# Kernel tuning notes

Hardware: AMD Instinct MI355X
Metric: run time of the kernel (lower is better)

Reference implementation:

```python
import jax, jax.numpy as jnp
import numpy as np

KH, KW, PAD, G = 3, 3, 1, 4  # kernel, padding, deformable groups


def _bilinear_gather(xg, py, px):
    """xg: [B,G,C,Hin,Win]; py,px: [B,G,K,H,W] sample coords.
    Returns [B,G,C,K,H,W] with zero padding outside the image (mmcv semantics)."""
    B, Gd, C, Hin, Win = xg.shape
    y0 = jnp.floor(py)
    x0 = jnp.floor(px)
    wy1 = py - y0
    wx1 = px - x0
    wy0 = 1.0 - wy1
    wx0 = 1.0 - wx1
    xf = xg.reshape(B, Gd, C, Hin * Win)

    def gather(yi, xi):
        valid = (yi >= 0) & (yi < Hin) & (xi >= 0) & (xi < Win)
        yc = jnp.clip(yi, 0, Hin - 1).astype(jnp.int32)
        xc = jnp.clip(xi, 0, Win - 1).astype(jnp.int32)
        lin = (yc * Win + xc).reshape(B, Gd, 1, -1)  # [B,G,1,K*H*W]
        v = jnp.take_along_axis(xf, lin, axis=3).reshape(B, Gd, C, *yi.shape[2:])
        return v * valid[:, :, None].astype(xg.dtype)

    return (gather(y0, x0) * (wy0 * wx0)[:, :, None]
            + gather(y0, x0 + 1) * (wy0 * wx1)[:, :, None]
            + gather(y0 + 1, x0) * (wy1 * wx0)[:, :, None]
            + gather(y0 + 1, x0 + 1) * (wy1 * wx1)[:, :, None])


def setup_inputs() -> dict:
    key = jax.random.key(0)
    k1, k2, k3, k4 = jax.random.split(key, 4)
    B, Cin, Cout, H, W = 8, 256, 256, 64, 64
    x = jax.random.normal(k1, (B, Cin, H, W), dtype=jnp.float32)
    shape = jax.random.normal(k2, (B, 4, H, W), dtype=jnp.float32)
    # conv_offset: 1x1 conv, 4 -> G*2*KH*KW = 72 channels, no bias
    w_offset = jax.random.normal(k3, (G * 2 * KH * KW, 4), dtype=jnp.float32) * 0.1
    # conv_adaption: deform conv weight, no bias
    w_deform = jax.random.normal(k4, (Cout, Cin, KH, KW), dtype=jnp.float32) * 0.01
    return {"x": x, "shape": shape, "w_offset": w_offset, "w_deform": w_deform}


def reference(x, shape, w_offset, w_deform):
    B, Cin, H, W = x.shape
    Cout = w_deform.shape[0]
    K = KH * KW
    # 1x1 offset-predicting conv on detached shape
    shape = jax.lax.stop_gradient(shape)
    offset = jnp.einsum('oc,bchw->bohw', w_offset, shape)  # [B, G*2*K, H, W]
    off = offset.reshape(B, G, K, 2, H, W)  # mmcv layout: (dy, dx) per tap
    dy, dx = off[:, :, :, 0], off[:, :, :, 1]  # [B,G,K,H,W]
    # base sampling grid for each kernel tap
    ky, kx = jnp.meshgrid(jnp.arange(KH), jnp.arange(KW), indexing='ij')
    ky = ky.reshape(-1)
    kx = kx.reshape(-1)
    base_y = (ky - PAD)[:, None, None] + jnp.arange(H)[None, :, None]  # [K,H,1]
    base_x = (kx - PAD)[:, None, None] + jnp.arange(W)[None, None, :]  # [K,1,W]
    py = base_y[None, None].astype(x.dtype) + dy  # [B,G,K,H,W]
    px = base_x[None, None].astype(x.dtype) + dx
    xg = x.reshape(B, G, Cin // G, H, W)
    sampled = _bilinear_gather(xg, py, px)  # [B,G,Cpg,K,H,W]
    wr = w_deform.reshape(Cout, G, Cin // G, K)
    out = jnp.einsum('ogck,bgckhw->bohw', wr, sampled)
    return jax.nn.relu(out)
```

## Files before the change

kernel.cpp:

```cpp
#include <hip/hip_runtime.h>
#include <hip/hip_bf16.h>


#define Bn   8
#define CIN  256
#define COUT 256
#define Hn   64
#define Wn   64
#define Gn   4
#define Kn   9
#define CPG  64
#define GK   36

typedef __bf16 bf16x8 __attribute__((ext_vector_type(8)));
typedef float  f32x4  __attribute__((ext_vector_type(4)));

__global__ void fa_prep(const float* __restrict__ x, const float* __restrict__ w,
                        __bf16* __restrict__ xt, __bf16* __restrict__ wfrag) {
    const int bid = blockIdx.x, t = threadIdx.x;
    if (bid < 4096) {
        const int c8q = bid & 7, hwt = (bid >> 3) & 63, b = bid >> 9;
        const int hw = hwt * 64 + (t & 63);
        const int c8 = c8q * 4 + (t >> 6);
        const float* xp = x + ((size_t)(b * CIN + c8 * 8) << 12) + hw;
        bf16x8 v;
#pragma unroll
        for (int j = 0; j < 8; j++) v[j] = (__bf16)xp[(size_t)j << 12];
        *(bf16x8*)&xt[(((size_t)b << 12) + hw) * 256 + c8 * 8] = v;
    } else {
        int i = (bid - 4096) * 256 + t;
        int j    = i & 7;
        int lane = (i >> 3) & 63;
        int ks   = (i >> 9) & 1;
        int mt   = (i >> 10) & 15;
        int gk   = i >> 14;
        int g = gk / Kn, k = gk - g * Kn;
        int o = mt * 16 + (lane & 15);
        int c = ks * 32 + (lane >> 4) * 8 + j;
        wfrag[i] = (__bf16)w[(size_t)(o * CIN + g * CPG + c) * Kn + k];
    }
}

__global__ __launch_bounds__(256, 2)
void fa_main(const __bf16* __restrict__ xt, const float* __restrict__ shp,
             const float* __restrict__ w_off, const __bf16* __restrict__ wfrag,
             float* __restrict__ out) {
    const int blk = blockIdx.x;
    const int bp = blk >> 7, h = (blk >> 1) & 63, wh = blk & 1;
    const int w0 = wh * 32;
    const int t = threadIdx.x;
    const int wid = t >> 6, lane = t & 63;
    const int col = lane & 15, quad = lane >> 4;
    const int cg = t & 7, nl0 = t >> 3;

    __shared__ int   s_iyx[GK * 64];
    __shared__ float s_fy[GK * 64];
    __shared__ float s_fx[GK * 64];
    __shared__ __align__(16) __bf16 sB[2][64 * 64];

    for (int i = t; i < GK * 64; i += 256) {
        int gk = i >> 6, n = i & 63;
        int bb = n >> 5, w = w0 + (n & 31);
        int b = bp * 2 + bb;
        int g = gk / Kn, k = gk - g * Kn;
        int ky = k / 3, kx = k - ky * 3;
        int oy = (g * Kn + k) * 2;
        float dy = 0.f, dx = 0.f;
#pragma unroll
        for (int c = 0; c < 4; c++) {
            float sv = shp[((b * 4 + c) * Hn + h) * Wn + w];
            dy = fmaf(w_off[(oy    ) * 4 + c], sv, dy);
            dx = fmaf(w_off[(oy + 1) * 4 + c], sv, dx);
        }
        float py = (float)(h + ky - 1) + dy;
        float px = (float)(w + kx - 1) + dx;
        float y0 = floorf(py), x0 = floorf(px);
        s_fy[i] = py - y0;
        s_fx[i] = px - x0;
        s_iyx[i] = (((int)y0 & 0xffff) << 16) | ((int)x0 & 0xffff);
    }

    bf16x8 c4[2][4];
    float  w4[2][4];

    auto issue = [&](int gk) {
#pragma unroll
        for (int s = 0; s < 2; s++) {
            int n = nl0 + s * 32;
            int bb = n >> 5;
            int b = bp * 2 + bb;
            int m = gk * 64 + n;
            int g = gk / Kn;
            int pk = s_iyx[m];
            int iy = pk >> 16, ix = (pk << 16) >> 16;
            float fy = s_fy[m], fx = s_fx[m];
            bool y0v = (unsigned)iy       < (unsigned)Hn;
            bool y1v = (unsigned)(iy + 1) < (unsigned)Hn;
            bool x0v = (unsigned)ix       < (unsigned)Wn;
            bool x1v = (unsigned)(ix + 1) < (unsigned)Wn;
            int yc0 = min(max(iy, 0), Hn - 1), yc1 = min(max(iy + 1, 0), Hn - 1);
            int xc0 = min(max(ix, 0), Wn - 1), xc1 = min(max(ix + 1, 0), Wn - 1);
            const __bf16* base = xt + (((size_t)b << 12)) * 256 + g * CPG + cg * 8;
            c4[s][0] = *(const bf16x8*)(base + ((size_t)(yc0 * 64 + xc0)) * 256);
            c4[s][1] = *(const bf16x8*)(base + ((size_t)(yc0 * 64 + xc1)) * 256);
            c4[s][2] = *(const bf16x8*)(base + ((size_t)(yc1 * 64 + xc0)) * 256);
            c4[s][3] = *(const bf16x8*)(base + ((size_t)(yc1 * 64 + xc1)) * 256);
            float wy1 = fy, wy0 = 1.f - fy, wx1 = fx, wx0 = 1.f - fx;
            w4[s][0] = (y0v && x0v) ? wy0 * wx0 : 0.f;
            w4[s][1] = (y0v && x1v) ? wy0 * wx1 : 0.f;
            w4[s][2] = (y1v && x0v) ? wy1 * wx0 : 0.f;
            w4[s][3] = (y1v && x1v) ? wy1 * wx1 : 0.f;
        }
    };
    auto commit = [&](int buf) {
#pragma unroll
        for (int s = 0; s < 2; s++) {
            int n = nl0 + s * 32;
            bf16x8 r;
#pragma unroll
            for (int j = 0; j < 8; j++) {
                float v = w4[s][0] * (float)c4[s][0][j] + w4[s][1] * (float)c4[s][1][j]
                        + w4[s][2] * (float)c4[s][2][j] + w4[s][3] * (float)c4[s][3][j];
                r[j] = (__bf16)v;
            }
            *(bf16x8*)&sB[buf][(n * 8 + (cg ^ (n & 7))) * 8] = r;
        }
    };

    f32x4 acc[4][4];
#pragma unroll
    for (int mt = 0; mt < 4; mt++)
#pragma unroll
        for (int nt = 0; nt < 4; nt++) acc[mt][nt] = (f32x4){0.f, 0.f, 0.f, 0.f};

    __syncthreads();

    issue(0);
    commit(0);
    issue(1);
    __syncthreads();

    for (int gk = 0; gk < GK; gk++) {
        const int buf = gk & 1;
        const __bf16* wbase = wfrag + (((size_t)gk * 16 + wid * 4) * 2) * 512;
        bf16x8 af[2][4];
#pragma unroll
        for (int ks = 0; ks < 2; ks++)
#pragma unroll
            for (int mt = 0; mt < 4; mt++)
                af[ks][mt] = *(const bf16x8*)(wbase + ((size_t)(mt * 2 + ks) * 64 + lane) * 8);
        if (gk + 1 < GK) commit(buf ^ 1);
        if (gk + 2 < GK) issue(gk + 2);
#pragma unroll
        for (int ks = 0; ks < 2; ks++) {
            bf16x8 bfv[4];
#pragma unroll
            for (int nt = 0; nt < 4; nt++) {
                int n = nt * 16 + col;
                int cq8 = ks * 4 + quad;
                bfv[nt] = *(const bf16x8*)&sB[buf][(n * 8 + (cq8 ^ (n & 7))) * 8];
            }
#pragma unroll
            for (int mt = 0; mt < 4; mt++)
#pragma unroll
                for (int nt = 0; nt < 4; nt++)
                    acc[mt][nt] = __builtin_amdgcn_mfma_f32_16x16x32_bf16(
                        af[ks][mt], bfv[nt], acc[mt][nt], 0, 0, 0);
        }
        __syncthreads();
    }

#pragma unroll
    for (int mt = 0; mt < 4; mt++)
#pragma unroll
        for (int r = 0; r < 4; r++) {
            int o = wid * 64 + mt * 16 + quad * 4 + r;
#pragma unroll
            for (int nt = 0; nt < 4; nt++) {
                int n = nt * 16 + col;
                int b = bp * 2 + (n >> 5);
                int w = w0 + (n & 31);
                out[(((size_t)(b * COUT + o)) << 12) + h * Wn + w] =
                    fmaxf(acc[mt][nt][r], 0.f);
            }
        }
}

extern "C" void kernel_launch(void* const* d_in, const int* in_sizes, int n_in,
                              void* d_out, int out_size, void* d_ws, size_t ws_size,
                              hipStream_t stream) {
    const float* x     = (const float*)d_in[0];
    const float* shp   = (const float*)d_in[1];
    const float* w_off = (const float*)d_in[2];
    const float* w_def = (const float*)d_in[3];
    float* out = (float*)d_out;
    __bf16* wfrag = (__bf16*)d_ws;
    __bf16* xt    = (__bf16*)((char*)d_ws + (2u << 20));

    fa_prep<<<4096 + 2304, 256, 0, stream>>>(x, w_def, xt, wfrag);
    fa_main<<<512, 256, 0, stream>>>(xt, shp, w_off, wfrag, out);
}
```

Measured before the change: 154.7 us.

## Stage weight reformat through LDS and prefetch A fragments one step ahead

The weight-fragment prep now uses 32 blocks that read rows of w_deform with coalesced float4 loads into shared memory. Each block then gathers the MFMA fragment layout from shared memory, replacing the old strided per-element global gathers spread over 2304 blocks. The main loop is unrolled by two with double-buffered A-fragment registers, so the weights for the next step load while the current MFMAs run. The cost is more register pressure in the main kernel and an added 37KB of shared memory in the prep kernel, which may reduce occupancy for the x-transpose blocks.

Measured after the change: 154.3 us. Within noise of the previous version (-0.3%).

```diff
diff --git a/kernel.cpp b/kernel.cpp
--- a/kernel.cpp
+++ b/kernel.cpp
@@ -15,9 +15,11 @@
 typedef __bf16 bf16x8 __attribute__((ext_vector_type(8)));
 typedef float  f32x4  __attribute__((ext_vector_type(4)));
 
+#define SWPAD 1156
 __global__ void fa_prep(const float* __restrict__ x, const float* __restrict__ w,
                         __bf16* __restrict__ xt, __bf16* __restrict__ wfrag) {
     const int bid = blockIdx.x, t = threadIdx.x;
+    __shared__ __bf16 sw[16 * SWPAD];
     if (bid < 4096) {
         const int c8q = bid & 7, hwt = (bid >> 3) & 63, b = bid >> 9;
         const int hw = hwt * 64 + (t & 63);
@@ -28,16 +30,33 @@
         for (int j = 0; j < 8; j++) v[j] = (__bf16)xp[(size_t)j << 12];
         *(bf16x8*)&xt[(((size_t)b << 12) + hw) * 256 + c8 * 8] = v;
     } else {
-        int i = (bid - 4096) * 256 + t;
-        int j    = i & 7;
-        int lane = (i >> 3) & 63;
-        int ks   = (i >> 9) & 1;
-        int mt   = (i >> 10) & 15;
-        int gk   = i >> 14;
-        int g = gk / Kn, k = gk - g * Kn;
-        int o = mt * 16 + (lane & 15);
-        int c = ks * 32 + (lane >> 4) * 8 + j;
-        wfrag[i] = (__bf16)w[(size_t)(o * CIN + g * CPG + c) * Kn + k];
+        const int mt = (bid - 4096) >> 1, gh = (bid - 4096) & 1;
+        const int o0 = mt * 16, g0 = gh * 2;
+        const int r = t >> 4, tr = t & 15;
+        const float* wp = w + (size_t)(o0 + r) * (CIN * Kn) + g0 * (CPG * Kn);
+#pragma unroll
+        for (int it = 0; it < 18; it++) {
+            int off = it * 64 + tr * 4;
+            float4 v = *(const float4*)(wp + off);
+            __bf16* d = &sw[r * SWPAD + off];
+            d[0] = (__bf16)v.x; d[1] = (__bf16)v.y;
+            d[2] = (__bf16)v.z; d[3] = (__bf16)v.w;
+        }
+        __syncthreads();
+#pragma unroll
+        for (int it = 0; it < 9; it++) {
+            int chunk = it * 256 + t;
+            int lane = chunk & 63, ks = (chunk >> 6) & 1, gkl = chunk >> 7;
+            int gl = gkl / Kn, k = gkl - gl * Kn;
+            int gk = g0 * Kn + gkl;
+            int ol = lane & 15;
+            int cbase = ks * 32 + (lane >> 4) * 8;
+            bf16x8 v;
+#pragma unroll
+            for (int j = 0; j < 8; j++)
+                v[j] = sw[ol * SWPAD + (gl * CPG + cbase + j) * Kn + k];
+            *(bf16x8*)&wfrag[(((size_t)gk * 16 + mt) * 2 + ks) * 512 + lane * 8] = v;
+        }
     }
 }
 
@@ -87,8 +106,7 @@
 #pragma unroll
         for (int s = 0; s < 2; s++) {
             int n = nl0 + s * 32;
-            int bb = n >> 5;
-            int b = bp * 2 + bb;
+            int b = bp * 2 + (n >> 5);
             int m = gk * 64 + n;
             int g = gk / Kn;
             int pk = s_iyx[m];
@@ -126,31 +144,22 @@
             *(bf16x8*)&sB[buf][(n * 8 + (cg ^ (n & 7))) * 8] = r;
         }
     };
-
-    f32x4 acc[4][4];
-#pragma unroll
-    for (int mt = 0; mt < 4; mt++)
-#pragma unroll
-        for (int nt = 0; nt < 4; nt++) acc[mt][nt] = (f32x4){0.f, 0.f, 0.f, 0.f};
-
-    __syncthreads();
-
-    issue(0);
-    commit(0);
-    issue(1);
-    __syncthreads();
-
-    for (int gk = 0; gk < GK; gk++) {
-        const int buf = gk & 1;
+    auto loadA = [&](int gk, bf16x8 af[2][4]) {
         const __bf16* wbase = wfrag + (((size_t)gk * 16 + wid * 4) * 2) * 512;
-        bf16x8 af[2][4];
 #pragma unroll
         for (int ks = 0; ks < 2; ks++)
 #pragma unroll
             for (int mt = 0; mt < 4; mt++)
                 af[ks][mt] = *(const bf16x8*)(wbase + ((size_t)(mt * 2 + ks) * 64 + lane) * 8);
-        if (gk + 1 < GK) commit(buf ^ 1);
-        if (gk + 2 < GK) issue(gk + 2);
+    };
+
+    f32x4 acc[4][4];
+#pragma unroll
+    for (int mt = 0; mt < 4; mt++)
+#pragma unroll
+        for (int nt = 0; nt < 4; nt++) acc[mt][nt] = (f32x4){0.f, 0.f, 0.f, 0.f};
+
+    auto domfma = [&](bf16x8 af[2][4], int buf) {
 #pragma unroll
         for (int ks = 0; ks < 2; ks++) {
             bf16x8 bfv[4];
@@ -167,6 +176,28 @@
                     acc[mt][nt] = __builtin_amdgcn_mfma_f32_16x16x32_bf16(
                         af[ks][mt], bfv[nt], acc[mt][nt], 0, 0, 0);
         }
+    };
+
+    bf16x8 afA[2][4], afB[2][4];
+
+    __syncthreads();
+
+    loadA(0, afA);
+    issue(0);
+    commit(0);
+    issue(1);
+    __syncthreads();
+
+    for (int gk = 0; gk < GK; gk += 2) {
+        loadA(gk + 1, afB);
+        commit(1);
+        if (gk + 2 < GK) issue(gk + 2);
+        domfma(afA, 0);
+        __syncthreads();
+        if (gk + 2 < GK) loadA(gk + 2, afA);
+        if (gk + 2 < GK) commit(0);
+        if (gk + 3 < GK) issue(gk + 3);
+        domfma(afB, 1);
         __syncthreads();
     }
 
@@ -197,6 +228,6 @@
     __bf16* wfrag = (__bf16*)d_ws;
     __bf16* xt    = (__bf16*)((char*)d_ws + (2u << 20));
 
-    fa_prep<<<4096 + 2304, 256, 0, stream>>>(x, w_def, xt, wfrag);
+    fa_prep<<<4096 + 32, 256, 0, stream>>>(x, w_def, xt, wfrag);
     fa_main<<<512, 256, 0, stream>>>(xt, shp, w_off, wfrag, out);
 }
```
